# Kernel tuning notes

Measured on AMD Instinct MI355X. Metric: run time of the kernel, lower is better.

The kernel has to match this reference:

```python
import jax, jax.numpy as jnp
from jax import lax
import numpy as np

N_CLUSTERS = 8
G_CLUSTERS = 2
D_DIM = 512
DN = ('NCHW', 'OIHW', 'NCHW')


def _conv(x, w, b):
    y = lax.conv_general_dilated(x, w, window_strides=(1, 1), padding='VALID',
                                 dimension_numbers=DN)
    return y + b[None, :, None, None]


def setup_inputs() -> dict:
    key = jax.random.key(0)
    ks = jax.random.split(key, 6)
    B, D, H, W = 32, D_DIM, 7, 250
    KG = N_CLUSTERS + G_CLUSTERS
    scale = 1.0 / np.sqrt(D * 7)
    return {
        'x': jax.random.normal(ks[0], (B, D, H, W), dtype=jnp.float32),
        'feat_w': jax.random.normal(ks[1], (D, D, 7, 1), dtype=jnp.float32) * scale,
        'feat_b': jax.random.normal(ks[2], (D,), dtype=jnp.float32) * 0.01,
        'assign_w': jax.random.normal(ks[3], (KG, D, 7, 1), dtype=jnp.float32) * scale,
        'assign_b': jax.random.normal(ks[4], (KG,), dtype=jnp.float32) * 0.01,
        'centroids': jax.random.uniform(ks[5], (D, KG), dtype=jnp.float32),
    }


def reference(x, feat_w, feat_b, assign_w, assign_b, centroids):
    # features branch: conv(7,1) + ReLU -> (B, D, H', W)
    feat = jnp.maximum(_conv(x, feat_w, feat_b), 0.0)
    # assignment branch: conv(7,1) -> softmax over clusters -> (B, K+G, H', W)
    soft = jax.nn.softmax(_conv(x, assign_w, assign_b), axis=1)
    # Fused VLAD aggregation (mathematically identical to
    # sum_hw soft[b,k,hw] * (feat[b,d,hw] - centroids[d,k]) without
    # materializing the (B,D,K+G,H',W) residual tensor):
    s_sum = soft.sum(axis=(-2, -1))                                # (B, K+G)
    agg = jnp.einsum('bkhw,bdhw->bdk', soft, feat)                 # (B, D, K+G)
    cluster_res = agg - centroids[None, :, :] * s_sum[:, None, :]  # (B, D, K+G)
    cluster_res = cluster_res[..., :N_CLUSTERS]                    # drop ghost clusters
    # L2 normalize over feature dim (torch F.normalize, eps=1e-12)
    norm = jnp.sqrt(jnp.sum(cluster_res * cluster_res, axis=1, keepdims=True))
    cluster_l2 = cluster_res / jnp.maximum(norm, 1e-12)
    # (B, D, K) -> (B, K, D) -> (B, K*D)
    out = jnp.swapaxes(cluster_l2, 1, 2).reshape(x.shape[0], N_CLUSTERS * D_DIM)
    return out
```

## Files before the change

kernel.cpp:

```cpp
#include <hip/hip_runtime.h>
#include <stdint.h>

typedef float f32x4 __attribute__((ext_vector_type(4)));
typedef __bf16 bf16x8 __attribute__((ext_vector_type(8)));
typedef unsigned short ushortx8 __attribute__((ext_vector_type(8)));

#define D_DIM 512
#define KGC 10
#define NCLU 8
#define BATCH 32
#define WPOS 250
#define WPAD 256
#define KDIM 3584
#define MROWS 522
#define MPAD 528
#define MBIG 640
#define BM 160
#define BN 128
#define NS 56
#define NT 64
#define KSG 56
#define XTILE 8192

__device__ __forceinline__ float bf2f(unsigned short u) {
  union { unsigned int i; float f; } v; v.i = ((unsigned int)u) << 16; return v.f;
}
__device__ __forceinline__ unsigned short f2bf(float f) {
  union { float f; unsigned int i; } v; v.f = f;
  unsigned int r = v.i + 0x7FFFu + ((v.i >> 16) & 1u);
  return (unsigned short)(r >> 16);
}

__device__ __forceinline__ void load_lds16(const void* g, void* l) {
  __builtin_amdgcn_global_load_lds(
      (const __attribute__((address_space(1))) void*)g,
      (__attribute__((address_space(3))) void*)l, 16, 0, 0);
}

__global__ __launch_bounds__(256) void prep2_kernel(
    const float* __restrict__ fw, const float* __restrict__ fb,
    const float* __restrict__ aw, const float* __restrict__ ab,
    const float* __restrict__ x,
    unsigned short* __restrict__ Wcat, float* __restrict__ bcat,
    unsigned short* __restrict__ XS) {
  const int bid = blockIdx.x;
  const int tid = threadIdx.x;
  if (bid < MBIG) {
    int r = bid;
    unsigned short* dst = Wcat + (size_t)r * KDIM;
    const float* src = (r < D_DIM) ? (fw + (size_t)r * KDIM)
                     : (r < MROWS) ? (aw + (size_t)(r - D_DIM) * KDIM)
                                   : nullptr;
    for (int i = tid; i < KDIM / 4; i += 256) {
      unsigned short o0 = 0, o1 = 0, o2 = 0, o3 = 0;
      if (src) {
        float4 v = ((const float4*)src)[i];
        o0 = f2bf(v.x); o1 = f2bf(v.y); o2 = f2bf(v.z); o3 = f2bf(v.w);
      }
      ushort4 o; o.x = o0; o.y = o1; o.z = o2; o.w = o3;
      ((ushort4*)dst)[i] = o;
    }
    if (tid == 0)
      bcat[r] = r < D_DIM ? fb[r] : (r < MROWS ? ab[r - D_DIM] : 0.f);
  } else {
    const int xt = bid - MBIG;
    const int nt = xt / KSG, ksg = xt - nt * KSG;
    unsigned short* tb = XS + (size_t)(nt * KSG + ksg) * XTILE;
#pragma unroll
    for (int i = 0; i < 4; i++) {
      const int L = tid + 256 * i;
      const int ks = L >> 9, nf = (L >> 6) & 7, lane = L & 63;
      const int fr = lane & 15, kg = lane >> 4;
      const int n = nt * 128 + nf * 16 + fr;
      const int b = n >> 8, col = n & 255;
      const int k0 = ksg * 64 + ks * 32 + kg * 8;
      const float* xp = x + ((size_t)b * KDIM + k0) * WPOS + col;
      ushortx8 pk;
      if (col < WPOS) {
#pragma unroll
        for (int e = 0; e < 8; e++) pk[e] = f2bf(xp[(size_t)e * WPOS]);
      } else {
#pragma unroll
        for (int e = 0; e < 8; e++) pk[e] = 0;
      }
      *(ushortx8*)&tb[(size_t)L * 8] = pk;
    }
  }
}

__global__ __launch_bounds__(512, 2) void gemm_fused(
    const unsigned short* __restrict__ XS, const unsigned short* __restrict__ Wcat,
    const float* __restrict__ bcat, unsigned short* __restrict__ Y) {
  __shared__ __align__(16) unsigned short Wl[4][BM * 64];
  const int tid = threadIdx.x;
  const int nt = blockIdx.x, mh = blockIdx.y;
  const int lane = tid & 63, wv = tid >> 6;
  const int wm = wv >> 2, wn = wv & 3;
  const int fr = lane & 15, kg = lane >> 4;
  const int sx = fr & 7;
  const unsigned short* Wg = Wcat + (size_t)mh * BM * KDIM;
  const unsigned short* xsb = XS + (size_t)nt * (KSG * XTILE) + (wn * 1024 + lane * 8);

  auto stageW = [&](int st, int buf) {
#pragma unroll
    for (int it = 0; it < 3; it++) {
      int s = (it < 2) ? it * 512 + tid : 1024 + (tid & 255);
      int row = s >> 3, p = s & 7;
      int blk = p ^ (row & 7);
      load_lds16(Wg + (size_t)row * KDIM + st * 64 + blk * 8, &Wl[buf][s * 8]);
    }
  };
  auto loadX = [&](int st, bf16x8& x0, bf16x8& x1, bf16x8& x2, bf16x8& x3) {
    const unsigned short* p = xsb + (size_t)st * XTILE;
    x0 = *(const bf16x8*)(p);
    x1 = *(const bf16x8*)(p + 512);
    x2 = *(const bf16x8*)(p + 4096);
    x3 = *(const bf16x8*)(p + 4096 + 512);
  };

  f32x4 acc[5][2];
  const f32x4 zero = {0.f, 0.f, 0.f, 0.f};
#pragma unroll
  for (int f = 0; f < 5; f++) { acc[f][0] = zero; acc[f][1] = zero; }

  auto compute = [&](const unsigned short* wb, bf16x8 b00, bf16x8 b01,
                     bf16x8 b10, bf16x8 b11) {
#pragma unroll
    for (int ks = 0; ks < 2; ks++) {
      bf16x8 b0 = ks ? b10 : b00;
      bf16x8 b1 = ks ? b11 : b01;
      const int off = ((ks * 4 + kg) ^ sx) * 8;
#pragma unroll
      for (int f = 0; f < 5; f++) {
        bf16x8 af = *(const bf16x8*)&wb[(wm * 80 + f * 16 + fr) * 64 + off];
        acc[f][0] = __builtin_amdgcn_mfma_f32_16x16x32_bf16(af, b0, acc[f][0], 0, 0, 0);
        acc[f][1] = __builtin_amdgcn_mfma_f32_16x16x32_bf16(af, b1, acc[f][1], 0, 0, 0);
      }
    }
  };

  bf16x8 xA0, xA1, xA2, xA3, xB0, xB1, xB2, xB3;
  bf16x8 xC0, xC1, xC2, xC3, xD0, xD1, xD2, xD3;

  stageW(0, 0); loadX(0, xA0, xA1, xA2, xA3);
  stageW(1, 1); loadX(1, xB0, xB1, xB2, xB3);

#define STEP(u, BUF, PBUF, CX0, CX1, CX2, CX3, PX0, PX1, PX2, PX3)           \
  {                                                                          \
    if ((u) + 1 < NS) { asm volatile("s_waitcnt vmcnt(7)" ::: "memory"); }   \
    else              { asm volatile("s_waitcnt vmcnt(0)" ::: "memory"); }   \
    __builtin_amdgcn_s_barrier();                                            \
    __builtin_amdgcn_sched_barrier(0);                                       \
    if ((u) + 2 < NS) {                                                      \
      stageW((u) + 2, PBUF);                                                 \
      loadX((u) + 2, PX0, PX1, PX2, PX3);                                    \
    }                                                                        \
    compute(Wl[BUF], CX0, CX1, CX2, CX3);                                    \
  }

  for (int t = 0; t < NS; t += 4) {
    STEP(t + 0, 0, 2, xA0, xA1, xA2, xA3, xC0, xC1, xC2, xC3);
    STEP(t + 1, 1, 3, xB0, xB1, xB2, xB3, xD0, xD1, xD2, xD3);
    STEP(t + 2, 2, 0, xC0, xC1, xC2, xC3, xA0, xA1, xA2, xA3);
    STEP(t + 3, 3, 1, xD0, xD1, xD2, xD3, xB0, xB1, xB2, xB3);
  }
#undef STEP

  const int bb = (nt * BN) >> 8;
  const int cbase = (nt * BN) & 255;
  unsigned short* Yb = Y + (size_t)bb * MPAD * WPAD;
#pragma unroll
  for (int f = 0; f < 5; f++) {
    const int m0 = mh * BM + wm * 80 + f * 16 + kg * 4;
#pragma unroll
    for (int nf = 0; nf < 2; nf++) {
      const int c = cbase + wn * 32 + nf * 16 + fr;
#pragma unroll
      for (int r = 0; r < 4; r++) {
        const int m = m0 + r;
        if (m < MPAD) {
          float v = acc[f][nf][r] + bcat[m];
          if (m < D_DIM) v = fmaxf(v, 0.f);
          Yb[(size_t)m * WPAD + c] = f2bf(v);
        }
      }
    }
  }
}

__global__ __launch_bounds__(512) void epi_kernel(
    const unsigned short* __restrict__ Y, const float* __restrict__ cent,
    float* __restrict__ out) {
  __shared__ float soft[WPAD];
  __shared__ float red[8];
  const int b = blockIdx.x >> 3, k = blockIdx.x & 7;
  const int tid = threadIdx.x;
  const unsigned short* Yb = Y + (size_t)b * MPAD * WPAD;

  float sv = 0.f;
  if (tid < WPOS) {
    float lg[KGC];
    float mx = -1e30f;
#pragma unroll
    for (int j = 0; j < KGC; j++) {
      lg[j] = bf2f(Yb[(size_t)(D_DIM + j) * WPAD + tid]);
      mx = fmaxf(mx, lg[j]);
    }
    float s = 0.f, ek = 0.f;
#pragma unroll
    for (int j = 0; j < KGC; j++) {
      float e = __expf(lg[j] - mx);
      s += e;
      if (j == k) ek = e;
    }
    sv = ek / s;
  }
  if (tid < WPAD) soft[tid] = sv;
  __syncthreads();

  float v = sv;
#pragma unroll
  for (int o = 32; o > 0; o >>= 1) v += __shfl_down(v, o, 64);
  if ((tid & 63) == 0) red[tid >> 6] = v;
  __syncthreads();
  float ssum = 0.f;
#pragma unroll
  for (int i = 0; i < 8; i++) ssum += red[i];

  float a[8];
#pragma unroll
  for (int u = 0; u < 8; u++) a[u] = 0.f;
  const unsigned short* row = Yb + (size_t)tid * WPAD;
  for (int w = 0; w < WPAD; w += 8) {
    ushortx8 f0 = *(const ushortx8*)(row + w);
    float4 s0 = *(const float4*)&soft[w];
    float4 s1 = *(const float4*)&soft[w + 4];
    a[0] += bf2f(f0[0]) * s0.x;
    a[1] += bf2f(f0[1]) * s0.y;
    a[2] += bf2f(f0[2]) * s0.z;
    a[3] += bf2f(f0[3]) * s0.w;
    a[4] += bf2f(f0[4]) * s1.x;
    a[5] += bf2f(f0[5]) * s1.y;
    a[6] += bf2f(f0[6]) * s1.z;
    a[7] += bf2f(f0[7]) * s1.w;
  }
  float asum = ((a[0] + a[1]) + (a[2] + a[3])) + ((a[4] + a[5]) + (a[6] + a[7]));
  float c = asum - cent[(size_t)tid * KGC + k] * ssum;

  __syncthreads();
  float q = c * c;
#pragma unroll
  for (int o = 32; o > 0; o >>= 1) q += __shfl_down(q, o, 64);
  if ((tid & 63) == 0) red[tid >> 6] = q;
  __syncthreads();
  float nsum = 0.f;
#pragma unroll
  for (int i = 0; i < 8; i++) nsum += red[i];
  float norm = sqrtf(nsum);
  float inv = 1.f / fmaxf(norm, 1e-12f);

  float* ob = out + (size_t)b * (NCLU * D_DIM) + (size_t)k * D_DIM;
  ob[tid] = c * inv;
}

extern "C" void kernel_launch(void* const* d_in, const int* in_sizes, int n_in,
                              void* d_out, int out_size, void* d_ws, size_t ws_size,
                              hipStream_t stream) {
  const float* x  = (const float*)d_in[0];
  const float* fw = (const float*)d_in[1];
  const float* fb = (const float*)d_in[2];
  const float* aw = (const float*)d_in[3];
  const float* ab = (const float*)d_in[4];
  const float* ce = (const float*)d_in[5];
  float* out = (float*)d_out;
  char* ws = (char*)d_ws;

  const size_t WC_BYTES = (size_t)MBIG * KDIM * 2;
  const size_t BC_BYTES = 4096;
  const size_t XS_BYTES = (size_t)NT * KSG * XTILE * 2;
  unsigned short* Wc = (unsigned short*)(ws);
  float*          bc = (float*)(ws + WC_BYTES);
  unsigned short* XSp= (unsigned short*)(ws + WC_BYTES + BC_BYTES);
  unsigned short* Yv = (unsigned short*)(ws + WC_BYTES + BC_BYTES + XS_BYTES);

  prep2_kernel<<<MBIG + NT * KSG, 256, 0, stream>>>(fw, fb, aw, ab, x, Wc, bc, XSp);
  gemm_fused<<<dim3(NT, 4), 512, 0, stream>>>(XSp, Wc, bc, Yv);
  epi_kernel<<<BATCH * NCLU, 512, 0, stream>>>(Yv, ce, out);
}
```

Measured before the change: 255.0 us.

## Compute assignment logits in prep kernel, shrink GEMM to 512 rows with 128x128 tiles

The 10 assignment-conv logit rows are no longer folded into the bf16 GEMM (previously padded to 640 rows). The prep kernel now stages an x tile transposed through LDS, computes fp32 partial logits per K-chunk into a workspace, and the epilogue sums the 56 partials before the softmax. The GEMM drops to exactly 512 rows with a BM=128 tile, a 4x2 wave layout, and a reworked double-buffered pipeline with s_setprio. This removes about 20% of the padded MFMA work and also coalesces the x reads in prep. In exchange it adds a partial-logit buffer of roughly 18 MB of extra traffic and a serial 56-step reduction in the epilogue.

```diff
diff --git a/kernel.cpp b/kernel.cpp
--- a/kernel.cpp
+++ b/kernel.cpp
@@ -13,13 +13,12 @@
 #define WPAD 256
 #define KDIM 3584
 #define MROWS 522
-#define MPAD 528
-#define MBIG 640
-#define BM 160
+#define BM 128
 #define BN 128
 #define NS 56
 #define NT 64
 #define KSG 56
+#define NTOT 8192
 #define XTILE 8192
 
 __device__ __forceinline__ float bf2f(unsigned short u) {
@@ -42,49 +41,71 @@
     const float* __restrict__ aw, const float* __restrict__ ab,
     const float* __restrict__ x,
     unsigned short* __restrict__ Wcat, float* __restrict__ bcat,
-    unsigned short* __restrict__ XS) {
+    unsigned short* __restrict__ XS, float* __restrict__ LGP) {
   const int bid = blockIdx.x;
   const int tid = threadIdx.x;
-  if (bid < MBIG) {
+  if (bid < MROWS) {
     int r = bid;
-    unsigned short* dst = Wcat + (size_t)r * KDIM;
-    const float* src = (r < D_DIM) ? (fw + (size_t)r * KDIM)
-                     : (r < MROWS) ? (aw + (size_t)(r - D_DIM) * KDIM)
-                                   : nullptr;
-    for (int i = tid; i < KDIM / 4; i += 256) {
-      unsigned short o0 = 0, o1 = 0, o2 = 0, o3 = 0;
-      if (src) {
+    if (r < D_DIM) {
+      unsigned short* dst = Wcat + (size_t)r * KDIM;
+      const float* src = fw + (size_t)r * KDIM;
+      for (int i = tid; i < KDIM / 4; i += 256) {
         float4 v = ((const float4*)src)[i];
-        o0 = f2bf(v.x); o1 = f2bf(v.y); o2 = f2bf(v.z); o3 = f2bf(v.w);
+        ushort4 o; o.x = f2bf(v.x); o.y = f2bf(v.y); o.z = f2bf(v.z); o.w = f2bf(v.w);
+        ((ushort4*)dst)[i] = o;
       }
-      ushort4 o; o.x = o0; o.y = o1; o.z = o2; o.w = o3;
-      ((ushort4*)dst)[i] = o;
-    }
-    if (tid == 0)
-      bcat[r] = r < D_DIM ? fb[r] : (r < MROWS ? ab[r - D_DIM] : 0.f);
-  } else {
-    const int xt = bid - MBIG;
-    const int nt = xt / KSG, ksg = xt - nt * KSG;
+    }
+    if (tid == 0) bcat[r] = (r < D_DIM) ? fb[r] : ab[r - D_DIM];
+    return;
+  }
+  __shared__ float Xt[64][130];
+  __shared__ float Awl[KGC * 64];
+  const int xt = bid - MROWS;
+  const int nt = xt / KSG, ksg = xt - nt * KSG;
+  const int b = nt >> 1, c0 = (nt & 1) * 128;
+  const int k0 = ksg * 64;
+  {
+    const int l2 = tid & 63, r0 = tid >> 6;
+#pragma unroll
+    for (int p = 0; p < 16; p++) {
+      const int row = r0 + p * 4;
+      const int gc = c0 + l2 * 2;
+      const float* xp = x + ((size_t)b * KDIM + k0 + row) * WPOS + gc;
+      float v0 = 0.f, v1 = 0.f;
+      if (gc + 1 < WPOS) { float2 v = *(const float2*)xp; v0 = v.x; v1 = v.y; }
+      else if (gc < WPOS) { v0 = xp[0]; }
+      Xt[row][l2 * 2] = v0;
+      Xt[row][l2 * 2 + 1] = v1;
+    }
+  }
+#pragma unroll
+  for (int i = 0; i < 3; i++) {
+    int q = tid + 256 * i;
+    if (q < KGC * 64) Awl[q] = aw[(size_t)(q >> 6) * KDIM + k0 + (q & 63)];
+  }
+  __syncthreads();
+  {
     unsigned short* tb = XS + (size_t)(nt * KSG + ksg) * XTILE;
 #pragma unroll
     for (int i = 0; i < 4; i++) {
       const int L = tid + 256 * i;
       const int ks = L >> 9, nf = (L >> 6) & 7, lane = L & 63;
       const int fr = lane & 15, kg = lane >> 4;
-      const int n = nt * 128 + nf * 16 + fr;
-      const int b = n >> 8, col = n & 255;
-      const int k0 = ksg * 64 + ks * 32 + kg * 8;
-      const float* xp = x + ((size_t)b * KDIM + k0) * WPOS + col;
       ushortx8 pk;
-      if (col < WPOS) {
-#pragma unroll
-        for (int e = 0; e < 8; e++) pk[e] = f2bf(xp[(size_t)e * WPOS]);
-      } else {
-#pragma unroll
-        for (int e = 0; e < 8; e++) pk[e] = 0;
-      }
+#pragma unroll
+      for (int e = 0; e < 8; e++)
+        pk[e] = f2bf(Xt[ks * 32 + kg * 8 + e][nf * 16 + fr]);
       *(ushortx8*)&tb[(size_t)L * 8] = pk;
     }
+  }
+#pragma unroll
+  for (int i = 0; i < 5; i++) {
+    const int idx = tid + 256 * i;
+    const int j = idx >> 7, c = idx & 127;
+    float s = 0.f;
+#pragma unroll 8
+    for (int kk = 0; kk < 64; kk++) s += Awl[j * 64 + kk] * Xt[kk][c];
+    LGP[((size_t)ksg * KGC + j) * NTOT + nt * 128 + c] = s;
   }
 }
 
@@ -95,117 +116,127 @@
   const int tid = threadIdx.x;
   const int nt = blockIdx.x, mh = blockIdx.y;
   const int lane = tid & 63, wv = tid >> 6;
-  const int wm = wv >> 2, wn = wv & 3;
+  const int wm = wv >> 1, wn = wv & 1;
   const int fr = lane & 15, kg = lane >> 4;
   const int sx = fr & 7;
   const unsigned short* Wg = Wcat + (size_t)mh * BM * KDIM;
-  const unsigned short* xsb = XS + (size_t)nt * (KSG * XTILE) + (wn * 1024 + lane * 8);
+  const unsigned short* xsb = XS + (size_t)nt * (KSG * XTILE) + (wn * 2048 + lane * 8);
 
   auto stageW = [&](int st, int buf) {
 #pragma unroll
-    for (int it = 0; it < 3; it++) {
-      int s = (it < 2) ? it * 512 + tid : 1024 + (tid & 255);
+    for (int it = 0; it < 2; it++) {
+      int s = it * 512 + tid;
       int row = s >> 3, p = s & 7;
       int blk = p ^ (row & 7);
       load_lds16(Wg + (size_t)row * KDIM + st * 64 + blk * 8, &Wl[buf][s * 8]);
     }
   };
-  auto loadX = [&](int st, bf16x8& x0, bf16x8& x1, bf16x8& x2, bf16x8& x3) {
-    const unsigned short* p = xsb + (size_t)st * XTILE;
-    x0 = *(const bf16x8*)(p);
-    x1 = *(const bf16x8*)(p + 512);
-    x2 = *(const bf16x8*)(p + 4096);
-    x3 = *(const bf16x8*)(p + 4096 + 512);
-  };
-
-  f32x4 acc[5][2];
+#define LOADX(st, XR)                                                        \
+  {                                                                          \
+    const unsigned short* p_ = xsb + (size_t)(st) * XTILE;                   \
+    XR[0] = *(const bf16x8*)(p_);                                            \
+    XR[1] = *(const bf16x8*)(p_ + 512);                                      \
+    XR[2] = *(const bf16x8*)(p_ + 1024);                                     \
+    XR[3] = *(const bf16x8*)(p_ + 1536);                                     \
+    XR[4] = *(const bf16x8*)(p_ + 4096);                                     \
+    XR[5] = *(const bf16x8*)(p_ + 4096 + 512);                               \
+    XR[6] = *(const bf16x8*)(p_ + 4096 + 1024);                              \
+    XR[7] = *(const bf16x8*)(p_ + 4096 + 1536);                              \
+  }
+
+  f32x4 acc[2][4];
   const f32x4 zero = {0.f, 0.f, 0.f, 0.f};
 #pragma unroll
-  for (int f = 0; f < 5; f++) { acc[f][0] = zero; acc[f][1] = zero; }
-
-  auto compute = [&](const unsigned short* wb, bf16x8 b00, bf16x8 b01,
-                     bf16x8 b10, bf16x8 b11) {
-#pragma unroll
-    for (int ks = 0; ks < 2; ks++) {
-      bf16x8 b0 = ks ? b10 : b00;
-      bf16x8 b1 = ks ? b11 : b01;
-      const int off = ((ks * 4 + kg) ^ sx) * 8;
-#pragma unroll
-      for (int f = 0; f < 5; f++) {
-        bf16x8 af = *(const bf16x8*)&wb[(wm * 80 + f * 16 + fr) * 64 + off];
-        acc[f][0] = __builtin_amdgcn_mfma_f32_16x16x32_bf16(af, b0, acc[f][0], 0, 0, 0);
-        acc[f][1] = __builtin_amdgcn_mfma_f32_16x16x32_bf16(af, b1, acc[f][1], 0, 0, 0);
-      }
-    }
-  };
-
-  bf16x8 xA0, xA1, xA2, xA3, xB0, xB1, xB2, xB3;
-  bf16x8 xC0, xC1, xC2, xC3, xD0, xD1, xD2, xD3;
-
-  stageW(0, 0); loadX(0, xA0, xA1, xA2, xA3);
-  stageW(1, 1); loadX(1, xB0, xB1, xB2, xB3);
-
-#define STEP(u, BUF, PBUF, CX0, CX1, CX2, CX3, PX0, PX1, PX2, PX3)           \
+  for (int f = 0; f < 2; f++)
+#pragma unroll
+    for (int j = 0; j < 4; j++) acc[f][j] = zero;
+
+#define COMPUTE(BUF, XR)                                                     \
   {                                                                          \
-    if ((u) + 1 < NS) { asm volatile("s_waitcnt vmcnt(7)" ::: "memory"); }   \
-    else              { asm volatile("s_waitcnt vmcnt(0)" ::: "memory"); }   \
-    __builtin_amdgcn_s_barrier();                                            \
-    __builtin_amdgcn_sched_barrier(0);                                       \
-    if ((u) + 2 < NS) {                                                      \
-      stageW((u) + 2, PBUF);                                                 \
-      loadX((u) + 2, PX0, PX1, PX2, PX3);                                    \
+    __builtin_amdgcn_s_setprio(1);                                           \
+    _Pragma("unroll")                                                        \
+    for (int ks = 0; ks < 2; ks++) {                                         \
+      const int off = ((ks * 4 + kg) ^ sx) * 8;                              \
+      _Pragma("unroll")                                                      \
+      for (int f = 0; f < 2; f++) {                                          \
+        bf16x8 af = *(const bf16x8*)&Wl[BUF][(wm * 32 + f * 16 + fr) * 64 + off]; \
+        acc[f][0] = __builtin_amdgcn_mfma_f32_16x16x32_bf16(af, XR[ks * 4 + 0], acc[f][0], 0, 0, 0); \
+        acc[f][1] = __builtin_amdgcn_mfma_f32_16x16x32_bf16(af, XR[ks * 4 + 1], acc[f][1], 0, 0, 0); \
+        acc[f][2] = __builtin_amdgcn_mfma_f32_16x16x32_bf16(af, XR[ks * 4 + 2], acc[f][2], 0, 0, 0); \
+        acc[f][3] = __builtin_amdgcn_mfma_f32_16x16x32_bf16(af, XR[ks * 4 + 3], acc[f][3], 0, 0, 0); \
+      }                                                                      \
     }                                                                        \
-    compute(Wl[BUF], CX0, CX1, CX2, CX3);                                    \
-  }
-
-  for (int t = 0; t < NS; t += 4) {
-    STEP(t + 0, 0, 2, xA0, xA1, xA2, xA3, xC0, xC1, xC2, xC3);
-    STEP(t + 1, 1, 3, xB0, xB1, xB2, xB3, xD0, xD1, xD2, xD3);
-    STEP(t + 2, 2, 0, xC0, xC1, xC2, xC3, xA0, xA1, xA2, xA3);
-    STEP(t + 3, 3, 1, xD0, xD1, xD2, xD3, xB0, xB1, xB2, xB3);
-  }
-#undef STEP
+    __builtin_amdgcn_s_setprio(0);                                           \
+  }
+
+  bf16x8 XA[8], XB[8];
+
+  stageW(0, 0);
+  stageW(1, 1);
+  LOADX(0, XA);
+
+  for (int t = 0; t < NS; t += 2) {
+    if (t + 2 < NS) stageW(t + 2, (t + 2) & 3);
+    LOADX(t + 1, XB);
+    if (t + 2 < NS) { asm volatile("s_waitcnt vmcnt(10)"); }
+    else            { asm volatile("s_waitcnt vmcnt(8)"); }
+    __builtin_amdgcn_s_barrier();
+    __builtin_amdgcn_sched_barrier(0);
+    COMPUTE((t) & 3, XA);
+    if (t + 3 < NS) stageW(t + 3, (t + 3) & 3);
+    if (t + 2 < NS) LOADX(t + 2, XA);
+    if (t + 3 < NS)      { asm volatile("s_waitcnt vmcnt(10)"); }
+    else if (t + 2 < NS) { asm volatile("s_waitcnt vmcnt(8)"); }
+    else                 { asm volatile("s_waitcnt vmcnt(0)"); }
+    __builtin_amdgcn_s_barrier();
+    __builtin_amdgcn_sched_barrier(0);
+    COMPUTE((t + 1) & 3, XB);
+  }
+#undef LOADX
+#undef COMPUTE
 
   const int bb = (nt * BN) >> 8;
   const int cbase = (nt * BN) & 255;
-  unsigned short* Yb = Y + (size_t)bb * MPAD * WPAD;
-#pragma unroll
-  for (int f = 0; f < 5; f++) {
-    const int m0 = mh * BM + wm * 80 + f * 16 + kg * 4;
-#pragma unroll
-    for (int nf = 0; nf < 2; nf++) {
-      const int c = cbase + wn * 32 + nf * 16 + fr;
-#pragma unroll
-      for (int r = 0; r < 4; r++) {
-        const int m = m0 + r;
-        if (m < MPAD) {
-          float v = acc[f][nf][r] + bcat[m];
-          if (m < D_DIM) v = fmaxf(v, 0.f);
-          Yb[(size_t)m * WPAD + c] = f2bf(v);
-        }
-      }
+  unsigned short* Yb = Y + (size_t)bb * D_DIM * WPAD;
+#pragma unroll
+  for (int f = 0; f < 2; f++) {
+    const int m0 = mh * BM + wm * 32 + f * 16 + kg * 4;
+    const float b0 = bcat[m0], b1 = bcat[m0 + 1], b2 = bcat[m0 + 2], b3 = bcat[m0 + 3];
+#pragma unroll
+    for (int j = 0; j < 4; j++) {
+      const int c = cbase + wn * 64 + j * 16 + fr;
+      Yb[(size_t)(m0 + 0) * WPAD + c] = f2bf(fmaxf(acc[f][j][0] + b0, 0.f));
+      Yb[(size_t)(m0 + 1) * WPAD + c] = f2bf(fmaxf(acc[f][j][1] + b1, 0.f));
+      Yb[(size_t)(m0 + 2) * WPAD + c] = f2bf(fmaxf(acc[f][j][2] + b2, 0.f));
+      Yb[(size_t)(m0 + 3) * WPAD + c] = f2bf(fmaxf(acc[f][j][3] + b3, 0.f));
     }
   }
 }
 
 __global__ __launch_bounds__(512) void epi_kernel(
-    const unsigned short* __restrict__ Y, const float* __restrict__ cent,
+    const unsigned short* __restrict__ Y, const float* __restrict__ LGP,
+    const float* __restrict__ bcat, const float* __restrict__ cent,
     float* __restrict__ out) {
   __shared__ float soft[WPAD];
   __shared__ float red[8];
   const int b = blockIdx.x >> 3, k = blockIdx.x & 7;
   const int tid = threadIdx.x;
-  const unsigned short* Yb = Y + (size_t)b * MPAD * WPAD;
+  const unsigned short* Yb = Y + (size_t)b * D_DIM * WPAD;
 
   float sv = 0.f;
   if (tid < WPOS) {
     float lg[KGC];
+#pragma unroll
+    for (int j = 0; j < KGC; j++) lg[j] = bcat[D_DIM + j];
+    const float* base = LGP + (size_t)b * 256 + tid;
+    for (int kq = 0; kq < KSG; kq++) {
+      const float* pp = base + (size_t)kq * KGC * NTOT;
+#pragma unroll
+      for (int j = 0; j < KGC; j++) lg[j] += pp[(size_t)j * NTOT];
+    }
     float mx = -1e30f;
 #pragma unroll
-    for (int j = 0; j < KGC; j++) {
-      lg[j] = bf2f(Yb[(size_t)(D_DIM + j) * WPAD + tid]);
-      mx = fmaxf(mx, lg[j]);
-    }
+    for (int j = 0; j < KGC; j++) mx = fmaxf(mx, lg[j]);
     float s = 0.f, ek = 0.f;
 #pragma unroll
     for (int j = 0; j < KGC; j++) {
@@ -275,15 +306,17 @@
   float* out = (float*)d_out;
   char* ws = (char*)d_ws;
 
-  const size_t WC_BYTES = (size_t)MBIG * KDIM * 2;
-  const size_t BC_BYTES = 4096;
-  const size_t XS_BYTES = (size_t)NT * KSG * XTILE * 2;
-  unsigned short* Wc = (unsigned short*)(ws);
-  float*          bc = (float*)(ws + WC_BYTES);
-  unsigned short* XSp= (unsigned short*)(ws + WC_BYTES + BC_BYTES);
-  unsigned short* Yv = (unsigned short*)(ws + WC_BYTES + BC_BYTES + XS_BYTES);
-
-  prep2_kernel<<<MBIG + NT * KSG, 256, 0, stream>>>(fw, fb, aw, ab, x, Wc, bc, XSp);
+  const size_t WC_BYTES  = (size_t)D_DIM * KDIM * 2;
+  const size_t BC_BYTES  = 4096;
+  const size_t XS_BYTES  = (size_t)NT * KSG * XTILE * 2;
+  const size_t LGP_BYTES = (size_t)KSG * KGC * NTOT * 4;
+  unsigned short* Wc  = (unsigned short*)(ws);
+  float*          bc  = (float*)(ws + WC_BYTES);
+  unsigned short* XSp = (unsigned short*)(ws + WC_BYTES + BC_BYTES);
+  float*          LGp = (float*)(ws + WC_BYTES + BC_BYTES + XS_BYTES);
+  unsigned short* Yv  = (unsigned short*)(ws + WC_BYTES + BC_BYTES + XS_BYTES + LGP_BYTES);
+
+  prep2_kernel<<<MROWS + NT * KSG, 256, 0, stream>>>(fw, fb, aw, ab, x, Wc, bc, XSp, LGp);
   gemm_fused<<<dim3(NT, 4), 512, 0, stream>>>(XSp, Wc, bc, Yv);
-  epi_kernel<<<BATCH * NCLU, 512, 0, stream>>>(Yv, ce, out);
-}
+  epi_kernel<<<BATCH * NCLU, 512, 0, stream>>>(Yv, LGp, bc, ce, out);
+}
```

After: 302.0 us. +18.4%, slower.
